# Kernel tuning notes

Measured on AMD Instinct MI355X. Metric: run time of the kernel, lower is better.

The kernel has to match this reference:

```python
import jax, jax.numpy as jnp
import numpy as np

E = 200_000   # edges (messages)
T = 2_000_000 # triplets
N = 20_000    # atoms/nodes
H = 128       # hidden_channels
INT = 64      # int_emb_size
BAS = 8       # basis_emb_size
OUT_EMB = 256 # out_emb_channels
NRAD = 6
SBF_DIM = 7 * 6  # num_spherical * num_radial = 42
NB = 4        # num_blocks
OUTC = 1      # num_targets


def setup_inputs() -> dict:
    key = jax.random.key(0)
    ks = iter(jax.random.split(key, 64))

    def w(shape):
        # glorot-ish scaled weights, stored as [in, out] for x @ W
        return jax.random.normal(next(ks), shape, jnp.float32) / np.sqrt(shape[-2])

    return dict(
        x=jax.random.normal(next(ks), (E, H), jnp.float32),
        rbf=jax.random.normal(next(ks), (E, NRAD), jnp.float32),
        sbf=jax.random.normal(next(ks), (T, SBF_DIM), jnp.float32),
        # interaction block params, stacked over NB blocks
        W_rbf1=w((NB, NRAD, BAS)), W_rbf2=w((NB, BAS, H)),
        W_sbf1=w((NB, SBF_DIM, BAS)), W_sbf2=w((NB, BAS, INT)),
        W_kj=w((NB, H, H)), b_kj=jnp.zeros((NB, H), jnp.float32),
        W_ji=w((NB, H, H)), b_ji=jnp.zeros((NB, H), jnp.float32),
        W_down=w((NB, H, INT)), W_up=w((NB, INT, H)),
        Wb=w((NB, 2, H, H)), bb=jnp.zeros((NB, 2, H), jnp.float32),   # num_before_skip=1 -> 2 linears
        Wa=w((NB, 4, H, H)), ba=jnp.zeros((NB, 4, H), jnp.float32),   # num_after_skip=2 -> 4 linears
        W_lin=w((NB, H, H)), b_lin=jnp.zeros((NB, H), jnp.float32),
        # output block params, stacked over NB+1 blocks
        Wo_rbf=w((NB + 1, NRAD, H)),
        Wo_up=w((NB + 1, H, OUT_EMB)), bo_up=jnp.zeros((NB + 1, OUT_EMB), jnp.float32),
        Wo_lins=w((NB + 1, 3, OUT_EMB, OUT_EMB)), bo_lins=jnp.zeros((NB + 1, 3, OUT_EMB), jnp.float32),
        Wo_out=w((NB + 1, OUT_EMB, OUTC)),
        idx_kj=jax.random.randint(next(ks), (T,), 0, E, jnp.int32),
        idx_ji=jax.random.randint(next(ks), (T,), 0, E, jnp.int32),
        idx_i=jax.random.randint(next(ks), (E,), 0, N, jnp.int32),
        num_nodes=N,
    )


def _interaction(b, x, rbf, sbf, idx_kj, idx_ji, p):
    act = jax.nn.silu
    x_ji = act(x @ p['W_ji'][b] + p['b_ji'][b])
    x_kj = act(x @ p['W_kj'][b] + p['b_kj'][b])
    rbf_t = (rbf @ p['W_rbf1'][b]) @ p['W_rbf2'][b]          # [E,H]
    x_kj = act((x_kj * rbf_t) @ p['W_down'][b])              # [E,INT]
    sbf_t = (sbf @ p['W_sbf1'][b]) @ p['W_sbf2'][b]          # [T,INT]
    m = x_kj[idx_kj] * sbf_t                                  # triplet gather [T,INT]
    agg = jax.ops.segment_sum(m, idx_ji, num_segments=x.shape[0])  # scatter-add [E,INT]
    x_kj = act(agg @ p['W_up'][b])                            # [E,H]
    h = x_ji + x_kj
    # residual layers before skip (1 layer = 2 linears)
    h = h + act(act(h @ p['Wb'][b, 0] + p['bb'][b, 0]) @ p['Wb'][b, 1] + p['bb'][b, 1])
    h = act(h @ p['W_lin'][b] + p['b_lin'][b]) + x
    # residual layers after skip (2 layers = 4 linears)
    for l in range(2):
        h = h + act(act(h @ p['Wa'][b, 2 * l] + p['ba'][b, 2 * l]) @ p['Wa'][b, 2 * l + 1] + p['ba'][b, 2 * l + 1])
    return h


def _output(b, x, rbf, idx_i, num_nodes, p):
    act = jax.nn.silu
    t = (rbf @ p['Wo_rbf'][b]) * x                            # [E,H]
    t = jax.ops.segment_sum(t, idx_i, num_segments=num_nodes) # [N,H]
    t = t @ p['Wo_up'][b] + p['bo_up'][b]
    for l in range(3):
        t = act(t @ p['Wo_lins'][b, l] + p['bo_lins'][b, l])
    return t @ p['Wo_out'][b]                                 # [N,OUTC]


def reference(x, rbf, sbf, W_rbf1, W_rbf2, W_sbf1, W_sbf2, W_kj, b_kj, W_ji, b_ji,
              W_down, W_up, Wb, bb, Wa, ba, W_lin, b_lin,
              Wo_rbf, Wo_up, bo_up, Wo_lins, bo_lins, Wo_out,
              idx_kj, idx_ji, idx_i, num_nodes):
    p = dict(W_rbf1=W_rbf1, W_rbf2=W_rbf2, W_sbf1=W_sbf1, W_sbf2=W_sbf2,
             W_kj=W_kj, b_kj=b_kj, W_ji=W_ji, b_ji=b_ji, W_down=W_down, W_up=W_up,
             Wb=Wb, bb=bb, Wa=Wa, ba=ba, W_lin=W_lin, b_lin=b_lin,
             Wo_rbf=Wo_rbf, Wo_up=Wo_up, bo_up=bo_up,
             Wo_lins=Wo_lins, bo_lins=bo_lins, Wo_out=Wo_out)
    P = _output(0, x, rbf, idx_i, num_nodes, p)
    for b in range(NB):  # fixed small layer loop
        x = _interaction(b, x, rbf, sbf, idx_kj, idx_ji, p)
        P = P + _output(b + 1, x, rbf, idx_i, num_nodes, p)
    return P
```

## Files before the change

### kernel.cpp

```cpp
#include <hip/hip_runtime.h>
#include <hip/hip_bf16.h>

#define E_EDGES 200000
#define T_TRIP  2000000
#define N_NODES 20000
#define H_DIM   128
#define INT_DIM 64
#define BAS     8
#define OUT_EMB 256
#define NRAD    6
#define SBF_D   42
#define NB      4

typedef __attribute__((ext_vector_type(8))) __bf16 bf16x8;
typedef __attribute__((ext_vector_type(4))) float f32x4;
typedef unsigned short u16;

__device__ __forceinline__ float silu_f(float v) { return v / (1.0f + __expf(-v)); }

__device__ __forceinline__ u16 f2bf(float f) {
    unsigned int u = __float_as_uint(f);
    u += 0x7FFF + ((u >> 16) & 1);
    return (u16)(u >> 16);
}
__device__ __forceinline__ float bf2f(u16 h) {
    return __uint_as_float(((unsigned int)h) << 16);
}

__device__ __forceinline__ void st_split4(char* H, char* L, int row, int col0, int stride,
                                          const float v[4]) {
    ushort4 hh, ll;
    u16 h0 = f2bf(v[0]); ll.x = f2bf(v[0] - bf2f(h0)); hh.x = h0;
    u16 h1 = f2bf(v[1]); ll.y = f2bf(v[1] - bf2f(h1)); hh.y = h1;
    u16 h2 = f2bf(v[2]); ll.z = f2bf(v[2] - bf2f(h2)); hh.z = h2;
    u16 h3 = f2bf(v[3]); ll.w = f2bf(v[3] - bf2f(h3)); hh.w = h3;
    int off = (row * stride + col0 * 2) ^ ((row & 7) << 4);
    *reinterpret_cast<ushort4*>(H + off) = hh;
    *reinterpret_cast<ushort4*>(L + off) = ll;
}
__device__ __forceinline__ void ld_split4(const char* H, const char* L, int row, int col0,
                                          int stride, float v[4]) {
    int off = (row * stride + col0 * 2) ^ ((row & 7) << 4);
    ushort4 hh = *reinterpret_cast<const ushort4*>(H + off);
    ushort4 ll = *reinterpret_cast<const ushort4*>(L + off);
    v[0] = bf2f(hh.x) + bf2f(ll.x);
    v[1] = bf2f(hh.y) + bf2f(ll.y);
    v[2] = bf2f(hh.z) + bf2f(ll.z);
    v[3] = bf2f(hh.w) + bf2f(ll.w);
}

struct BF8x4 { bf16x8 h[4]; bf16x8 l[4]; };

__device__ __forceinline__ BF8x4 loadB128f(const u16* __restrict__ Bh, const u16* __restrict__ Bl,
                                           int k0, int wn, int l15, int khalf)
{
    BF8x4 f;
    #pragma unroll
    for (int n = 0; n < 4; ++n) {
        size_t bo = (size_t)(wn * 64 + n * 16 + l15) * 128 + k0 + khalf;
        f.h[n] = *reinterpret_cast<const bf16x8*>(Bh + bo);
        f.l[n] = *reinterpret_cast<const bf16x8*>(Bl + bo);
    }
    return f;
}
__device__ __forceinline__ BF8x4 loadB64f(const u16* __restrict__ Bh, const u16* __restrict__ Bl,
                                          int k0, int wn, int l15, int khalf)
{
    BF8x4 f;
    #pragma unroll
    for (int n = 0; n < 4; ++n) {
        size_t bo = (size_t)(wn * 64 + n * 16 + l15) * 64 + k0 + khalf;
        f.h[n] = *reinterpret_cast<const bf16x8*>(Bh + bo);
        f.l[n] = *reinterpret_cast<const bf16x8*>(Bl + bo);
    }
    return f;
}
__device__ __forceinline__ BF8x4 loadB256f(const u16* __restrict__ Bh, const u16* __restrict__ Bl,
                                           int k0, int wn, int l15, int khalf)
{
    BF8x4 f;
    #pragma unroll
    for (int n = 0; n < 4; ++n) {
        size_t bo = (size_t)(wn * 64 + n * 16 + l15) * 256 + k0 + khalf;
        f.h[n] = *reinterpret_cast<const bf16x8*>(Bh + bo);
        f.l[n] = *reinterpret_cast<const bf16x8*>(Bl + bo);
    }
    return f;
}

__device__ __forceinline__ void mfma_cluster(
    const char* AH, const char* AL, int k0, int wm, int l15, int khalf,
    const BF8x4& b, f32x4 acc[2][4])
{
    __builtin_amdgcn_s_setprio(1);
    #pragma unroll
    for (int m = 0; m < 2; ++m) {
        int row = wm * 32 + m * 16 + l15;
        int off = (row * 256 + (k0 + khalf) * 2) ^ ((row & 7) << 4);
        bf16x8 ah = *reinterpret_cast<const bf16x8*>(AH + off);
        bf16x8 al = *reinterpret_cast<const bf16x8*>(AL + off);
        #pragma unroll
        for (int n = 0; n < 4; ++n) {
            acc[m][n] = __builtin_amdgcn_mfma_f32_16x16x32_bf16(b.h[n], ah, acc[m][n], 0, 0, 0);
            acc[m][n] = __builtin_amdgcn_mfma_f32_16x16x32_bf16(b.h[n], al, acc[m][n], 0, 0, 0);
            acc[m][n] = __builtin_amdgcn_mfma_f32_16x16x32_bf16(b.l[n], ah, acc[m][n], 0, 0, 0);
        }
    }
    __builtin_amdgcn_s_setprio(0);
}
__device__ __forceinline__ void mfma_cluster64(
    const char* AH, const char* AL, int k0, int wm, int l15, int khalf,
    const BF8x4& b, f32x4 acc[2][4])
{
    __builtin_amdgcn_s_setprio(1);
    #pragma unroll
    for (int m = 0; m < 2; ++m) {
        int row = wm * 32 + m * 16 + l15;
        int off = (row * 128 + (k0 + khalf) * 2) ^ ((row & 7) << 4);
        bf16x8 ah = *reinterpret_cast<const bf16x8*>(AH + off);
        bf16x8 al = *reinterpret_cast<const bf16x8*>(AL + off);
        #pragma unroll
        for (int n = 0; n < 4; ++n) {
            acc[m][n] = __builtin_amdgcn_mfma_f32_16x16x32_bf16(b.h[n], ah, acc[m][n], 0, 0, 0);
            acc[m][n] = __builtin_amdgcn_mfma_f32_16x16x32_bf16(b.h[n], al, acc[m][n], 0, 0, 0);
            acc[m][n] = __builtin_amdgcn_mfma_f32_16x16x32_bf16(b.l[n], ah, acc[m][n], 0, 0, 0);
        }
    }
    __builtin_amdgcn_s_setprio(0);
}
__device__ __forceinline__ void mfma_cluster512(
    const char* AH, const char* AL, int k0, int l15, int khalf,
    const BF8x4& b, f32x4 acc[2][4])
{
    __builtin_amdgcn_s_setprio(1);
    #pragma unroll
    for (int m = 0; m < 2; ++m) {
        int row = m * 16 + l15;
        int off = (row * 512 + (k0 + khalf) * 2) ^ ((row & 7) << 4);
        bf16x8 ah = *reinterpret_cast<const bf16x8*>(AH + off);
        bf16x8 al = *reinterpret_cast<const bf16x8*>(AL + off);
        #pragma unroll
        for (int n = 0; n < 4; ++n) {
            acc[m][n] = __builtin_amdgcn_mfma_f32_16x16x32_bf16(b.h[n], ah, acc[m][n], 0, 0, 0);
            acc[m][n] = __builtin_amdgcn_mfma_f32_16x16x32_bf16(b.h[n], al, acc[m][n], 0, 0, 0);
            acc[m][n] = __builtin_amdgcn_mfma_f32_16x16x32_bf16(b.l[n], ah, acc[m][n], 0, 0, 0);
        }
    }
    __builtin_amdgcn_s_setprio(0);
}

__device__ __forceinline__ void mm128_pipe(
    const char* AH, const char* AL,
    const u16* __restrict__ Bh, const u16* __restrict__ Bl, BF8x4& pre,
    const u16* __restrict__ nBh, const u16* __restrict__ nBl,
    int wm, int wn, int l15, int khalf, f32x4 acc[2][4])
{
    BF8x4 c0 = pre;
    BF8x4 c1 = loadB128f(Bh, Bl, 32, wn, l15, khalf);
    mfma_cluster(AH, AL, 0, wm, l15, khalf, c0, acc);
    BF8x4 c2 = loadB128f(Bh, Bl, 64, wn, l15, khalf);
    mfma_cluster(AH, AL, 32, wm, l15, khalf, c1, acc);
    BF8x4 c3 = loadB128f(Bh, Bl, 96, wn, l15, khalf);
    mfma_cluster(AH, AL, 64, wm, l15, khalf, c2, acc);
    if (nBh) pre = loadB128f(nBh, nBl, 0, wn, l15, khalf);
    mfma_cluster(AH, AL, 96, wm, l15, khalf, c3, acc);
}
__device__ __forceinline__ void mm64_pipe(
    const char* AH, const char* AL,
    const u16* __restrict__ Bh, const u16* __restrict__ Bl, BF8x4& pre,
    const u16* __restrict__ nBh, const u16* __restrict__ nBl,
    int wm, int wn, int l15, int khalf, f32x4 acc[2][4])
{
    BF8x4 c0 = pre;
    BF8x4 c1 = loadB64f(Bh, Bl, 32, wn, l15, khalf);
    mfma_cluster64(AH, AL, 0, wm, l15, khalf, c0, acc);
    if (nBh) pre = loadB128f(nBh, nBl, 0, wn, l15, khalf);
    mfma_cluster64(AH, AL, 32, wm, l15, khalf, c1, acc);
}

__global__ __launch_bounds__(256) void wprep(
    const float* __restrict__ src, u16* __restrict__ hi,
    u16* __restrict__ lo, int K, int N)
{
    int e = blockIdx.x * 256 + threadIdx.x;
    int total = K * N;
    if (e >= total) return;
    size_t base = (size_t)blockIdx.y * total;
    float a = src[base + e];
    int k = e / N, n = e - k * N;
    u16 h = f2bf(a);
    u16 l = f2bf(a - bf2f(h));
    hi[base + (size_t)n * K + k] = h;
    lo[base + (size_t)n * K + k] = l;
}

__global__ __launch_bounds__(256, 2) void pre_fuse(
    const float* __restrict__ X, const float* __restrict__ R8,
    const u16* __restrict__ Wjih, const u16* __restrict__ Wjil, const float* __restrict__ bji,
    const u16* __restrict__ Wkjh, const u16* __restrict__ Wkjl, const float* __restrict__ bkj,
    const float* __restrict__ Wr2,
    const u16* __restrict__ Wdnh, const u16* __restrict__ Wdnl,
    float* __restrict__ E1, float* __restrict__ C1)
{
    __shared__ u16 XH[64 * 128], XL[64 * 128];
    __shared__ u16 IH[64 * 128], IL[64 * 128];

    const int tid  = threadIdx.x;
    const int lane = tid & 63;
    const int w    = tid >> 6;
    const int wm   = w >> 1, wn = w & 1;
    const int bm   = blockIdx.x * 64;
    const int l15  = lane & 15;
    const int khalf = (lane >> 4) * 8;
    const int r4   = (lane >> 4) * 4;

    BF8x4 pre = loadB128f(Wjih, Wjil, 0, wn, l15, khalf);

    {
        int r  = tid >> 2;
        int c0 = (tid & 3) * 32;
        const float* p = &X[(size_t)(bm + r) * H_DIM + c0];
        const int swz = (r & 7) << 4;
        #pragma unroll
        for (int q = 0; q < 8; ++q) {
            float4 f = *reinterpret_cast<const float4*>(p + q * 4);
            float vv[4] = {f.x, f.y, f.z, f.w};
            u16 h[4], l[4];
            #pragma unroll
            for (int j = 0; j < 4; ++j) {
                h[j] = f2bf(vv[j]);
                l[j] = f2bf(vv[j] - bf2f(h[j]));
            }
            int off = (r * 256 + c0 * 2 + q * 8) ^ swz;
            *reinterpret_cast<ushort4*>((char*)XH + off) = make_ushort4(h[0], h[1], h[2], h[3]);
            *reinterpret_cast<ushort4*>((char*)XL + off) = make_ushort4(l[0], l[1], l[2], l[3]);
        }
    }
    __syncthreads();

    {
        f32x4 acc[2][4] = {};
        mm128_pipe((char*)XH, (char*)XL, Wjih, Wjil, pre, Wkjh, Wkjl,
                   wm, wn, l15, khalf, acc);
        #pragma unroll
        for (int n = 0; n < 4; ++n) {
            int col0 = wn * 64 + n * 16 + r4;
            float4 bv = *reinterpret_cast<const float4*>(&bji[col0]);
            #pragma unroll
            for (int m = 0; m < 2; ++m) {
                int row = wm * 32 + m * 16 + l15;
                float4 o;
                o.x = silu_f(acc[m][n][0] + bv.x);
                o.y = silu_f(acc[m][n][1] + bv.y);
                o.z = silu_f(acc[m][n][2] + bv.z);
                o.w = silu_f(acc[m][n][3] + bv.w);
                *reinterpret_cast<float4*>(&E1[(size_t)(bm + row) * H_DIM + col0]) = o;
            }
        }
    }
    {
        f32x4 acc[2][4] = {};
        mm128_pipe((char*)XH, (char*)XL, Wkjh, Wkjl, pre, nullptr, nullptr,
                   wm, wn, l15, khalf, acc);
        float r8v[2][8];
        #pragma unroll
        for (int m = 0; m < 2; ++m) {
            int grow = bm + wm * 32 + m * 16 + l15;
            const float4* rp = reinterpret_cast<const float4*>(&R8[(size_t)grow * 8]);
            float4 a = rp[0], b2 = rp[1];
            r8v[m][0] = a.x;  r8v[m][1] = a.y;  r8v[m][2] = a.z;  r8v[m][3] = a.w;
            r8v[m][4] = b2.x; r8v[m][5] = b2.y; r8v[m][6] = b2.z; r8v[m][7] = b2.w;
        }
        #pragma unroll
        for (int n = 0; n < 4; ++n) {
            int col0 = wn * 64 + n * 16 + r4;
            float4 bvf = *reinterpret_cast<const float4*>(&bkj[col0]);
            float bv[4] = {bvf.x, bvf.y, bvf.z, bvf.w};
            float wrv[8][4];
            #pragma unroll
            for (int j = 0; j < 8; ++j) {
                float4 wf = *reinterpret_cast<const float4*>(&Wr2[j * H_DIM + col0]);
                wrv[j][0] = wf.x; wrv[j][1] = wf.y; wrv[j][2] = wf.z; wrv[j][3] = wf.w;
            }
            #pragma unroll
            for (int m = 0; m < 2; ++m) {
                int row = wm * 32 + m * 16 + l15;
                float v[4];
                #pragma unroll
                for (int r = 0; r < 4; ++r) {
                    float t = silu_f(acc[m][n][r] + bv[r]);
                    float g = 0.f;
                    #pragma unroll
                    for (int j = 0; j < 8; ++j)
                        g = fmaf(r8v[m][j], wrv[j][r], g);
                    v[r] = t * g;
                }
                st_split4((char*)IH, (char*)IL, row, col0, 256, v);
            }
        }
    }
    __syncthreads();

    {
        f32x4 acc[2][2] = {};
        #pragma unroll
        for (int k0 = 0; k0 < 128; k0 += 32) {
            bf16x8 bh[2], bl[2];
            #pragma unroll
            for (int n = 0; n < 2; ++n) {
                size_t bo = (size_t)(wn * 32 + n * 16 + l15) * 128 + k0 + khalf;
                bh[n] = *reinterpret_cast<const bf16x8*>(Wdnh + bo);
                bl[n] = *reinterpret_cast<const bf16x8*>(Wdnl + bo);
            }
            __builtin_amdgcn_s_setprio(1);
            #pragma unroll
            for (int m = 0; m < 2; ++m) {
                int row = wm * 32 + m * 16 + l15;
                int off = (row * 256 + (k0 + khalf) * 2) ^ ((row & 7) << 4);
                bf16x8 ah = *reinterpret_cast<const bf16x8*>((const char*)IH + off);
                bf16x8 al = *reinterpret_cast<const bf16x8*>((const char*)IL + off);
                #pragma unroll
                for (int n = 0; n < 2; ++n) {
                    acc[m][n] = __builtin_amdgcn_mfma_f32_16x16x32_bf16(bh[n], ah, acc[m][n], 0, 0, 0);
                    acc[m][n] = __builtin_amdgcn_mfma_f32_16x16x32_bf16(bh[n], al, acc[m][n], 0, 0, 0);
                    acc[m][n] = __builtin_amdgcn_mfma_f32_16x16x32_bf16(bl[n], ah, acc[m][n], 0, 0, 0);
                }
            }
            __builtin_amdgcn_s_setprio(0);
        }
        #pragma unroll
        for (int n = 0; n < 2; ++n) {
            int col0 = wn * 32 + n * 16 + r4;
            #pragma unroll
            for (int m = 0; m < 2; ++m) {
                int row = wm * 32 + m * 16 + l15;
                float4 o;
                o.x = silu_f(acc[m][n][0]);
                o.y = silu_f(acc[m][n][1]);
                o.z = silu_f(acc[m][n][2]);
                o.w = silu_f(acc[m][n][3]);
                *reinterpret_cast<float4*>(&C1[(size_t)(bm + row) * INT_DIM + col0]) = o;
            }
        }
    }
}

struct ChainP {
    const u16 *uph, *upl;
    const u16 *b0h, *b0l, *b1h, *b1l;
    const u16 *lnh, *lnl;
    const u16 *a0h, *a0l, *a1h, *a1l, *a2h, *a2l, *a3h, *a3l;
    const float *bb0, *bb1, *blin, *ba0, *ba1, *ba2, *ba3;
};

__global__ __launch_bounds__(256, 2) void post_chain(
    const float* __restrict__ AGG, const float* __restrict__ E1,
    const float* __restrict__ X, ChainP p, float* __restrict__ OUT)
{
    __shared__ u16 GH[64 * 64],  GL[64 * 64];
    __shared__ u16 P0H[64 * 128], P0L[64 * 128];
    __shared__ u16 P1H[64 * 128], P1L[64 * 128];

    const int tid  = threadIdx.x;
    const int lane = tid & 63;
    const int w    = tid >> 6;
    const int wm   = w >> 1, wn = w & 1;
    const int bm   = blockIdx.x * 64;
    const int l15  = lane & 15;
    const int khalf = (lane >> 4) * 8;
    const int r4   = (lane >> 4) * 4;

    BF8x4 pre = loadB64f(p.uph, p.upl, 0, wn, l15, khalf);

    {
        int r  = tid >> 2;
        int c0 = (tid & 3) * 16;
        const float* pg = &AGG[(size_t)(bm + r) * INT_DIM + c0];
        const int swz = (r & 7) << 4;
        #pragma unroll
        for (int q = 0; q < 4; ++q) {
            float4 f = *reinterpret_cast<const float4*>(pg + q * 4);
            float vv[4] = {f.x, f.y, f.z, f.w};
            u16 h[4], l[4];
            #pragma unroll
            for (int j = 0; j < 4; ++j) {
                h[j] = f2bf(vv[j]);
                l[j] = f2bf(vv[j] - bf2f(h[j]));
            }
            int off = (r * 128 + c0 * 2 + q * 8) ^ swz;
            *reinterpret_cast<ushort4*>((char*)GH + off) = make_ushort4(h[0], h[1], h[2], h[3]);
            *reinterpret_cast<ushort4*>((char*)GL + off) = make_ushort4(l[0], l[1], l[2], l[3]);
        }
    }
    __syncthreads();

    f32x4 acc[2][4];

    #pragma unroll
    for (int m = 0; m < 2; ++m)
        #pragma unroll
        for (int n = 0; n < 4; ++n) acc[m][n] = f32x4{0.f, 0.f, 0.f, 0.f};
    mm64_pipe((char*)GH, (char*)GL, p.uph, p.upl, pre, p.b0h, p.b0l,
              wm, wn, l15, khalf, acc);
    #pragma unroll
    for (int n = 0; n < 4; ++n) {
        int col0 = wn * 64 + n * 16 + r4;
        #pragma unroll
        for (int m = 0; m < 2; ++m) {
            int row = wm * 32 + m * 16 + l15;
            float4 e = *reinterpret_cast<const float4*>(&E1[(size_t)(bm + row) * H_DIM + col0]);
            float v[4];
            v[0] = e.x + silu_f(acc[m][n][0]);
            v[1] = e.y + silu_f(acc[m][n][1]);
            v[2] = e.z + silu_f(acc[m][n][2]);
            v[3] = e.w + silu_f(acc[m][n][3]);
            st_split4((char*)P0H, (char*)P0L, row, col0, 256, v);
        }
    }
    __syncthreads();

    #define STAGE_PLAIN(SRC_H, SRC_L, WH, WL, BIAS, DST_H, DST_L, NWH, NWL)             \
    {                                                                                   \
        _Pragma("unroll")                                                               \
        for (int m = 0; m < 2; ++m)                                                     \
            _Pragma("unroll")                                                           \
            for (int n = 0; n < 4; ++n) acc[m][n] = f32x4{0.f, 0.f, 0.f, 0.f};          \
        mm128_pipe((char*)SRC_H, (char*)SRC_L, WH, WL, pre, NWH, NWL,                   \
                   wm, wn, l15, khalf, acc);                                            \
        _Pragma("unroll")                                                               \
        for (int n = 0; n < 4; ++n) {                                                   \
            int col0 = wn * 64 + n * 16 + r4;                                           \
            float4 bv = *reinterpret_cast<const float4*>(&BIAS[col0]);                  \
            _Pragma("unroll")                                                           \
            for (int m = 0; m < 2; ++m) {                                               \
                int row = wm * 32 + m * 16 + l15;                                       \
                float v[4];                                                             \
                v[0] = silu_f(acc[m][n][0] + bv.x);                                     \
                v[1] = silu_f(acc[m][n][1] + bv.y);                                     \
                v[2] = silu_f(acc[m][n][2] + bv.z);                                     \
                v[3] = silu_f(acc[m][n][3] + bv.w);                                     \
                st_split4((char*)DST_H, (char*)DST_L, row, col0, 256, v);               \
            }                                                                           \
        }                                                                               \
        __syncthreads();                                                                \
    }

    #define STAGE_RES(SRC_H, SRC_L, WH, WL, BIAS, RES_H, RES_L, NWH, NWL)               \
    {                                                                                   \
        _Pragma("unroll")                                                               \
        for (int m = 0; m < 2; ++m)                                                     \
            _Pragma("unroll")                                                           \
            for (int n = 0; n < 4; ++n) acc[m][n] = f32x4{0.f, 0.f, 0.f, 0.f};          \
        mm128_pipe((char*)SRC_H, (char*)SRC_L, WH, WL, pre, NWH, NWL,                   \
                   wm, wn, l15, khalf, acc);                                            \
        _Pragma("unroll")                                                               \
        for (int n = 0; n < 4; ++n) {                                                   \
            int col0 = wn * 64 + n * 16 + r4;                                           \
            float4 bv = *reinterpret_cast<const float4*>(&BIAS[col0]);                  \
            _Pragma("unroll")                                                           \
            for (int m = 0; m < 2; ++m) {                                               \
                int row = wm * 32 + m * 16 + l15;                                       \
                float v[4];                                                             \
                ld_split4((char*)RES_H, (char*)RES_L, row, col0, 256, v);               \
                v[0] += silu_f(acc[m][n][0] + bv.x);                                    \
                v[1] += silu_f(acc[m][n][1] + bv.y);                                    \
                v[2] += silu_f(acc[m][n][2] + bv.z);                                    \
                v[3] += silu_f(acc[m][n][3] + bv.w);                                    \
                st_split4((char*)RES_H, (char*)RES_L, row, col0, 256, v);               \
            }                                                                           \
        }                                                                               \
        __syncthreads();                                                                \
    }

    STAGE_PLAIN(P0H, P0L, p.b0h, p.b0l, p.bb0, P1H, P1L, p.b1h, p.b1l)
    STAGE_RES(P1H, P1L, p.b1h, p.b1l, p.bb1, P0H, P0L, p.lnh, p.lnl)

    {
        #pragma unroll
        for (int m = 0; m < 2; ++m)
            #pragma unroll
            for (int n = 0; n < 4; ++n) acc[m][n] = f32x4{0.f, 0.f, 0.f, 0.f};
        mm128_pipe((char*)P0H, (char*)P0L, p.lnh, p.lnl, pre, p.a0h, p.a0l,
                   wm, wn, l15, khalf, acc);
        #pragma unroll
        for (int n = 0; n < 4; ++n) {
            int col0 = wn * 64 + n * 16 + r4;
            float4 bv = *reinterpret_cast<const float4*>(&p.blin[col0]);
            #pragma unroll
            for (int m = 0; m < 2; ++m) {
                int row = wm * 32 + m * 16 + l15;
                float4 xv = *reinterpret_cast<const float4*>(&X[(size_t)(bm + row) * H_DIM + col0]);
                float v[4];
                v[0] = silu_f(acc[m][n][0] + bv.x) + xv.x;
                v[1] = silu_f(acc[m][n][1] + bv.y) + xv.y;
                v[2] = silu_f(acc[m][n][2] + bv.z) + xv.z;
                v[3] = silu_f(acc[m][n][3] + bv.w) + xv.w;
                st_split4((char*)P1H, (char*)P1L, row, col0, 256, v);
            }
        }
        __syncthreads();
    }

    STAGE_PLAIN(P1H, P1L, p.a0h, p.a0l, p.ba0, P0H, P0L, p.a1h, p.a1l)
    STAGE_RES(P0H, P0L, p.a1h, p.a1l, p.ba1, P1H, P1L, p.a2h, p.a2l)
    STAGE_PLAIN(P1H, P1L, p.a2h, p.a2l, p.ba2, P0H, P0L, p.a3h, p.a3l)

    {
        #pragma unroll
        for (int m = 0; m < 2; ++m)
            #pragma unroll
            for (int n = 0; n < 4; ++n) acc[m][n] = f32x4{0.f, 0.f, 0.f, 0.f};
        mm128_pipe((char*)P0H, (char*)P0L, p.a3h, p.a3l, pre, nullptr, nullptr,
                   wm, wn, l15, khalf, acc);
        #pragma unroll
        for (int n = 0; n < 4; ++n) {
            int col0 = wn * 64 + n * 16 + r4;
            float4 bv = *reinterpret_cast<const float4*>(&p.ba3[col0]);
            #pragma unroll
            for (int m = 0; m < 2; ++m) {
                int row = wm * 32 + m * 16 + l15;
                float v[4];
                ld_split4((char*)P1H, (char*)P1L, row, col0, 256, v);
                float4 o;
                o.x = v[0] + silu_f(acc[m][n][0] + bv.x);
                o.y = v[1] + silu_f(acc[m][n][1] + bv.y);
                o.z = v[2] + silu_f(acc[m][n][2] + bv.z);
                o.w = v[3] + silu_f(acc[m][n][3] + bv.w);
                *reinterpret_cast<float4*>(&OUT[(size_t)(bm + row) * H_DIM + col0]) = o;
            }
        }
    }
    #undef STAGE_PLAIN
    #undef STAGE_RES
}

__global__ __launch_bounds__(256, 2) void out_chain(
    const float* __restrict__ TN,
    const u16* __restrict__ Uh, const u16* __restrict__ Ul, const float* __restrict__ bu,
    const u16* __restrict__ L0h, const u16* __restrict__ L0l, const float* __restrict__ b0,
    const u16* __restrict__ L1h, const u16* __restrict__ L1l, const float* __restrict__ b1,
    const u16* __restrict__ L2h, const u16* __restrict__ L2l, const float* __restrict__ b2,
    const float* __restrict__ Wo, float* __restrict__ P)
{
    __shared__ u16 XH[32 * 128], XL[32 * 128];
    __shared__ u16 T0H[32 * 256], T0L[32 * 256];
    __shared__ u16 T1H[32 * 256], T1L[32 * 256];

    const int tid  = threadIdx.x;
    const int lane = tid & 63;
    const int wn   = tid >> 6;
    const int bm   = blockIdx.x * 32;
    const int l15  = lane & 15;
    const int khalf = (lane >> 4) * 8;
    const int r4   = (lane >> 4) * 4;

    {
        int r  = tid >> 3;
        int c0 = (tid & 7) * 16;
        const float* p = &TN[(size_t)(bm + r) * H_DIM + c0];
        const int swz = (r & 7) << 4;
        #pragma unroll
        for (int q = 0; q < 4; ++q) {
            float4 f = *reinterpret_cast<const float4*>(p + q * 4);
            float vv[4] = {f.x, f.y, f.z, f.w};
            u16 h[4], l[4];
            #pragma unroll
            for (int j = 0; j < 4; ++j) {
                h[j] = f2bf(vv[j]);
                l[j] = f2bf(vv[j] - bf2f(h[j]));
            }
            int off = (r * 256 + c0 * 2 + q * 8) ^ swz;
            *reinterpret_cast<ushort4*>((char*)XH + off) = make_ushort4(h[0], h[1], h[2], h[3]);
            *reinterpret_cast<ushort4*>((char*)XL + off) = make_ushort4(l[0], l[1], l[2], l[3]);
        }
    }
    __syncthreads();

    f32x4 acc[2][4];

    {
        #pragma unroll
        for (int m = 0; m < 2; ++m)
            #pragma unroll
            for (int n = 0; n < 4; ++n) acc[m][n] = f32x4{0.f, 0.f, 0.f, 0.f};
        BF8x4 cur = loadB128f(Uh, Ul, 0, wn, l15, khalf);
        #pragma unroll
        for (int k = 0; k < 4; ++k) {
            BF8x4 nxt;
            if (k < 3) nxt = loadB128f(Uh, Ul, 32 * (k + 1), wn, l15, khalf);
            mfma_cluster((char*)XH, (char*)XL, 32 * k, 0, l15, khalf, cur, acc);
            if (k < 3) cur = nxt;
        }
        #pragma unroll
        for (int n = 0; n < 4; ++n) {
            int col0 = wn * 64 + n * 16 + r4;
            float4 bv = *reinterpret_cast<const float4*>(&bu[col0]);
            #pragma unroll
            for (int m = 0; m < 2; ++m) {
                int row = m * 16 + l15;
                float v[4] = {acc[m][n][0] + bv.x, acc[m][n][1] + bv.y,
                              acc[m][n][2] + bv.z, acc[m][n][3] + bv.w};
                st_split4((char*)T0H, (char*)T0L, row, col0, 512, v);
            }
        }
        __syncthreads();
    }

    #define OLIN(SRC_H, SRC_L, WH, WL, BIAS, DST_H, DST_L)                              \
    {                                                                                   \
        _Pragma("unroll")                                                               \
        for (int m = 0; m < 2; ++m)                                                     \
            _Pragma("unroll")                                                           \
            for (int n = 0; n < 4; ++n) acc[m][n] = f32x4{0.f, 0.f, 0.f, 0.f};          \
        BF8x4 cur = loadB256f(WH, WL, 0, wn, l15, khalf);                               \
        _Pragma("unroll")                                                               \
        for (int k = 0; k < 8; ++k) {                                                   \
            BF8x4 nxt;                                                                  \
            if (k < 7) nxt = loadB256f(WH, WL, 32 * (k + 1), wn, l15, khalf);           \
            mfma_cluster512((char*)SRC_H, (char*)SRC_L, 32 * k, l15, khalf, cur, acc);  \
            if (k < 7) cur = nxt;                                                       \
        }                                                                               \
        _Pragma("unroll")                                                               \
        for (int n = 0; n < 4; ++n) {                                                   \
            int col0 = wn * 64 + n * 16 + r4;                                           \
            float4 bv = *reinterpret_cast<const float4*>(&BIAS[col0]);                  \
            _Pragma("unroll")                                                           \
            for (int m = 0; m < 2; ++m) {                                               \
                int row = m * 16 + l15;                                                 \
                float v[4];                                                             \
                v[0] = silu_f(acc[m][n][0] + bv.x);                                     \
                v[1] = silu_f(acc[m][n][1] + bv.y);                                     \
                v[2] = silu_f(acc[m][n][2] + bv.z);                                     \
                v[3] = silu_f(acc[m][n][3] + bv.w);                                     \
                st_split4((char*)DST_H, (char*)DST_L, row, col0, 512, v);               \
            }                                                                           \
        }                                                                               \
        __syncthreads();                                                                \
    }

    OLIN(T0H, T0L, L0h, L0l, b0, T1H, T1L)
    OLIN(T1H, T1L, L1h, L1l, b1, T0H, T0L)
    OLIN(T0H, T0L, L2h, L2l, b2, T1H, T1L)
    #undef OLIN

    {
        int row  = tid >> 3;
        int part = tid & 7;
        float s = 0.f;
        int cbase = part * 32;
        #pragma unroll
        for (int c4 = 0; c4 < 32; c4 += 4) {
            float v[4];
            ld_split4((char*)T1H, (char*)T1L, row, cbase + c4, 512, v);
            float4 wv = *reinterpret_cast<const float4*>(&Wo[cbase + c4]);
            s = fmaf(v[0], wv.x, s);
            s = fmaf(v[1], wv.y, s);
            s = fmaf(v[2], wv.z, s);
            s = fmaf(v[3], wv.w, s);
        }
        s += __shfl_xor(s, 1);
        s += __shfl_xor(s, 2);
        s += __shfl_xor(s, 4);
        if (part == 0) P[bm + row] += s;
    }
}

__global__ __launch_bounds__(256) void rbf8_kernel(
    const float* __restrict__ rbf, const float* __restrict__ W1,
    float* __restrict__ r8, int Ecount)
{
    int e = blockIdx.x * blockDim.x + threadIdx.x;
    if (e >= Ecount) return;
    float rv[NRAD];
    #pragma unroll
    for (int k = 0; k < NRAD; ++k) rv[k] = rbf[(size_t)e * NRAD + k];
    float acc[BAS] = {};
    #pragma unroll
    for (int k = 0; k < NRAD; ++k)
        #pragma unroll
        for (int j = 0; j < BAS; ++j)
            acc[j] = fmaf(rv[k], W1[k * BAS + j], acc[j]);
    float4* o = reinterpret_cast<float4*>(&r8[(size_t)e * BAS]);
    o[0] = make_float4(acc[0], acc[1], acc[2], acc[3]);
    o[1] = make_float4(acc[4], acc[5], acc[6], acc[7]);
}

__global__ __launch_bounds__(256) void csr_count(
    const int* __restrict__ idx, int* __restrict__ cnt, int n)
{
    int i = blockIdx.x * 256 + threadIdx.x;
    if (i < n) atomicAdd(&cnt[idx[i]], 1);
}

__global__ __launch_bounds__(256) void scan_block(
    const int* __restrict__ cnt, int* __restrict__ ptr, int* __restrict__ bsum, int n)
{
    __shared__ int s[256];
    int i = blockIdx.x * 256 + threadIdx.x;
    int v = (i < n) ? cnt[i] : 0;
    s[threadIdx.x] = v;
    __syncthreads();
    #pragma unroll
    for (int off = 1; off < 256; off <<= 1) {
        int t = (threadIdx.x >= off) ? s[threadIdx.x - off] : 0;
        __syncthreads();
        s[threadIdx.x] += t;
        __syncthreads();
    }
    if (i < n) ptr[i] = s[threadIdx.x] - v;
    if (threadIdx.x == 255) bsum[blockIdx.x] = s[255];
}

__global__ __launch_bounds__(1024) void scan_aux(int* __restrict__ bsum, int nb)
{
    __shared__ int s[1024];
    int v = (threadIdx.x < nb) ? bsum[threadIdx.x] : 0;
    s[threadIdx.x] = v;
    __syncthreads();
    #pragma unroll
    for (int off = 1; off < 1024; off <<= 1) {
        int t = (threadIdx.x >= off) ? s[threadIdx.x - off] : 0;
        __syncthreads();
        s[threadIdx.x] += t;
        __syncthreads();
    }
    if (threadIdx.x < nb) bsum[threadIdx.x] = s[threadIdx.x] - v;
}

__global__ __launch_bounds__(256) void scan_add(
    int* __restrict__ ptr, const int* __restrict__ bsum, int n)
{
    int i = blockIdx.x * 256 + threadIdx.x;
    if (i < n) ptr[i] += bsum[blockIdx.x];
}

__global__ __launch_bounds__(256) void csr_fill(
    const int* __restrict__ idx, int* __restrict__ cursor,
    int* __restrict__ perm, int n)
{
    int i = blockIdx.x * 256 + threadIdx.x;
    if (i >= n) return;
    int pos = atomicAdd(&cursor[idx[i]], 1);
    perm[pos] = i;
}

__global__ __launch_bounds__(256) void permute_s8(
    const float* __restrict__ sbf, const float* __restrict__ W1all,
    const int* __restrict__ idx_kj, const int* __restrict__ tperm,
    u16* __restrict__ ps8, int* __restrict__ pkj, int Tcount)
{
    __shared__ float Ws[NB * SBF_D * BAS];
    for (int i = threadIdx.x; i < NB * SBF_D * BAS; i += 256) Ws[i] = W1all[i];
    __syncthreads();
    int i = blockIdx.x * 256 + threadIdx.x;
    if (i >= Tcount) return;
    int t = tperm[i];
    pkj[i] = idx_kj[t];
    float s[SBF_D];
    {
        const float2* p2 = reinterpret_cast<const float2*>(&sbf[(size_t)t * SBF_D]);
        #pragma unroll
        for (int k = 0; k < SBF_D / 2; ++k) {
            float2 v = p2[k];
            s[2 * k] = v.x; s[2 * k + 1] = v.y;
        }
    }
    #pragma unroll
    for (int b = 0; b < NB; ++b) {
        const float* Wb_ = &Ws[b * SBF_D * BAS];
        float acc[BAS] = {};
        for (int k = 0; k < SBF_D; ++k) {
            float sv = s[k];
            #pragma unroll
            for (int j = 0; j < BAS; ++j)
                acc[j] = fmaf(sv, Wb_[k * BAS + j], acc[j]);
        }
        ushort4 o0 = make_ushort4(f2bf(acc[0]), f2bf(acc[1]), f2bf(acc[2]), f2bf(acc[3]));
        ushort4 o1 = make_ushort4(f2bf(acc[4]), f2bf(acc[5]), f2bf(acc[6]), f2bf(acc[7]));
        u16* op = &ps8[((size_t)b * Tcount + i) * BAS];
        *reinterpret_cast<ushort4*>(op) = o0;
        *reinterpret_cast<ushort4*>(op + 4) = o1;
    }
}

__device__ __forceinline__ float dot8_bf(uint4 r, const float* w2) {
    float s;
    s  = bf2f((u16)(r.x)) * w2[0] + bf2f((u16)(r.x >> 16)) * w2[1];
    s += bf2f((u16)(r.y)) * w2[2] + bf2f((u16)(r.y >> 16)) * w2[3];
    s += bf2f((u16)(r.z)) * w2[4] + bf2f((u16)(r.z >> 16)) * w2[5];
    s += bf2f((u16)(r.w)) * w2[6] + bf2f((u16)(r.w >> 16)) * w2[7];
    return s;
}

__global__ __launch_bounds__(256) void triplet_gather2(
    const u16* __restrict__ ps8b, const float* __restrict__ Wsb2,
    const float* __restrict__ xkj, const int* __restrict__ pkj,
    const int* __restrict__ tptr, const int* __restrict__ tcnt,
    float* __restrict__ agg, int Ecount)
{
    const int lane = threadIdx.x & 63;
    int wid = (blockIdx.x * blockDim.x + threadIdx.x) >> 6;
    const int nw = (gridDim.x * blockDim.x) >> 6;
    float w2[BAS];
    #pragma unroll
    for (int j = 0; j < BAS; ++j) w2[j] = Wsb2[j * INT_DIM + lane];

    for (int e = wid; e < Ecount; e += nw) {
        int start = tptr[e];
        int end   = start + tcnt[e];
        float acc0 = 0.f, acc1 = 0.f;
        int i = start;
        for (; i + 1 < end; i += 2) {
            uint4 ra = *reinterpret_cast<const uint4*>(&ps8b[(size_t)i * BAS]);
            uint4 rb = *reinterpret_cast<const uint4*>(&ps8b[(size_t)(i + 1) * BAS]);
            int e0 = pkj[i], e1 = pkj[i + 1];
            float s0 = dot8_bf(ra, w2);
            float s1 = dot8_bf(rb, w2);
            acc0 = fmaf(xkj[(size_t)e0 * INT_DIM + lane], s0, acc0);
            acc1 = fmaf(xkj[(size_t)e1 * INT_DIM + lane], s1, acc1);
        }
        if (i < end) {
            uint4 ra = *reinterpret_cast<const uint4*>(&ps8b[(size_t)i * BAS]);
            int e0 = pkj[i];
            acc0 = fmaf(xkj[(size_t)e0 * INT_DIM + lane], dot8_bf(ra, w2), acc0);
        }
        agg[(size_t)e * INT_DIM + lane] = acc0 + acc1;
    }
}

__global__ __launch_bounds__(256) void out_gather(
    const float* __restrict__ rbf, const float* __restrict__ Wor,
    const float* __restrict__ x,
    const int* __restrict__ eptr, const int* __restrict__ ecnt,
    const int* __restrict__ eperm, float* __restrict__ tN, int Nn)
{
    const int lane = threadIdx.x & 63;
    int wid = (blockIdx.x * blockDim.x + threadIdx.x) >> 6;
    const int nw = (gridDim.x * blockDim.x) >> 6;
    float wr0[NRAD], wr1[NRAD];
    #pragma unroll
    for (int k = 0; k < NRAD; ++k) {
        wr0[k] = Wor[k * H_DIM + lane];
        wr1[k] = Wor[k * H_DIM + lane + 64];
    }
    for (int n = wid; n < Nn; n += nw) {
        int start = eptr[n];
        int end   = start + ecnt[n];
        float a0 = 0.f, a1 = 0.f;
        for (int i = start; i < end; ++i) {
            int e = eperm[i];
            const float2* rp = reinterpret_cast<const float2*>(&rbf[(size_t)e * NRAD]);
            float2 r0 = rp[0], r1 = rp[1], r2 = rp[2];
            float rA = r0.x*wr0[0] + r0.y*wr0[1] + r1.x*wr0[2]
                     + r1.y*wr0[3] + r2.x*wr0[4] + r2.y*wr0[5];
            float rB = r0.x*wr1[0] + r0.y*wr1[1] + r1.x*wr1[2]
                     + r1.y*wr1[3] + r2.x*wr1[4] + r2.y*wr1[5];
            a0 = fmaf(rA, x[(size_t)e * H_DIM + lane], a0);
            a1 = fmaf(rB, x[(size_t)e * H_DIM + lane + 64], a1);
        }
        tN[(size_t)n * H_DIM + lane] = a0;
        tN[(size_t)n * H_DIM + lane + 64] = a1;
    }
}

extern "C" void kernel_launch(void* const* d_in, const int* in_sizes, int n_in,
                              void* d_out, int out_size, void* d_ws, size_t ws_size,
                              hipStream_t stream)
{
    const float* x_in    = (const float*)d_in[0];
    const float* rbf     = (const float*)d_in[1];
    const float* sbf     = (const float*)d_in[2];
    const float* W_rbf1  = (const float*)d_in[3];
    const float* W_rbf2  = (const float*)d_in[4];
    const float* W_sbf1  = (const float*)d_in[5];
    const float* W_sbf2  = (const float*)d_in[6];
    const float* W_kj    = (const float*)d_in[7];
    const float* b_kj    = (const float*)d_in[8];
    const float* W_ji    = (const float*)d_in[9];
    const float* b_ji    = (const float*)d_in[10];
    const float* W_down  = (const float*)d_in[11];
    const float* W_up    = (const float*)d_in[12];
    const float* Wb      = (const float*)d_in[13];
    const float* bb      = (const float*)d_in[14];
    const float* Wa      = (const float*)d_in[15];
    const float* ba      = (const float*)d_in[16];
    const float* W_lin   = (const float*)d_in[17];
    const float* b_lin   = (const float*)d_in[18];
    const float* Wo_rbf  = (const float*)d_in[19];
    const float* Wo_up   = (const float*)d_in[20];
    const float* bo_up   = (const float*)d_in[21];
    const float* Wo_lins = (const float*)d_in[22];
    const float* bo_lins = (const float*)d_in[23];
    const float* Wo_out  = (const float*)d_in[24];
    const int*   idx_kj  = (const int*)d_in[25];
    const int*   idx_ji  = (const int*)d_in[26];
    const int*   idx_i   = (const int*)d_in[27];

    char* ws = (char*)d_ws;
    size_t off = 0;
    auto alloc = [&](size_t bytes) -> void* {
        void* p = (void*)(ws + off);
        off += (bytes + 255) & ~(size_t)255;
        return p;
    };
    float* XA = (float*)alloc((size_t)E_EDGES * H_DIM * 4);
    float* XB = (float*)alloc((size_t)E_EDGES * H_DIM * 4);
    float* E1 = (float*)alloc((size_t)E_EDGES * H_DIM * 4);
    float* C1 = (float*)alloc((size_t)E_EDGES * INT_DIM * 4);
    float* C2 = (float*)alloc((size_t)E_EDGES * INT_DIM * 4);
    float* R8 = (float*)alloc((size_t)E_EDGES * BAS * 4);
    float* TN = (float*)alloc((size_t)N_NODES * H_DIM * 4);
    u16* HKJ = (u16*)alloc(4  * 16384 * 2); u16* LKJ = (u16*)alloc(4  * 16384 * 2);
    u16* HJI = (u16*)alloc(4  * 16384 * 2); u16* LJI = (u16*)alloc(4  * 16384 * 2);
    u16* HDN = (u16*)alloc(4  * 8192  * 2); u16* LDN = (u16*)alloc(4  * 8192  * 2);
    u16* HUP = (u16*)alloc(4  * 8192  * 2); u16* LUP = (u16*)alloc(4  * 8192  * 2);
    u16* HWB = (u16*)alloc(8  * 16384 * 2); u16* LWB = (u16*)alloc(8  * 16384 * 2);
    u16* HWA = (u16*)alloc(16 * 16384 * 2); u16* LWA = (u16*)alloc(16 * 16384 * 2);
    u16* HLN = (u16*)alloc(4  * 16384 * 2); u16* LLN = (u16*)alloc(4  * 16384 * 2);
    u16* HOU = (u16*)alloc(5  * 32768 * 2); u16* LOU = (u16*)alloc(5  * 32768 * 2);
    u16* HOL = (u16*)alloc(15 * 65536 * 2); u16* LOL = (u16*)alloc(15 * 65536 * 2);
    int* tcnt  = (int*)alloc((size_t)E_EDGES * 4);
    int* tptr  = (int*)alloc((size_t)E_EDGES * 4);
    int* tcur  = (int*)alloc((size_t)E_EDGES * 4);
    int* tperm = (int*)alloc((size_t)T_TRIP * 4);
    int* tbsum = (int*)alloc(1024 * 4);
    int* ecnt  = (int*)alloc((size_t)N_NODES * 4);
    int* eptr  = (int*)alloc((size_t)N_NODES * 4);
    int* ecur  = (int*)alloc((size_t)N_NODES * 4);
    int* eperm = (int*)alloc((size_t)E_EDGES * 4);
    int* ebsum = (int*)alloc(1024 * 4);
    u16* PS8 = (u16*)alloc((size_t)NB * T_TRIP * BAS * 2);
    int* PKJ = (int*)alloc((size_t)T_TRIP * 4);
    (void)ws_size;

    auto prep = [&](const float* src, u16* hi, u16* lo, int K, int N, int cnt) {
        dim3 g((K * N + 255) / 256, cnt);
        hipLaunchKernelGGL(wprep, g, dim3(256), 0, stream, src, hi, lo, K, N);
    };
    prep(W_kj,    HKJ, LKJ, 128, 128, 4);
    prep(W_ji,    HJI, LJI, 128, 128, 4);
    prep(W_down,  HDN, LDN, 128, 64,  4);
    prep(W_up,    HUP, LUP, 64,  128, 4);
    prep(Wb,      HWB, LWB, 128, 128, 8);
    prep(Wa,      HWA, LWA, 128, 128, 16);
    prep(W_lin,   HLN, LLN, 128, 128, 4);
    prep(Wo_up,   HOU, LOU, 128, 256, 5);
    prep(Wo_lins, HOL, LOL, 256, 256, 15);

    {
        const int nbT = (E_EDGES + 255) / 256;
        hipMemsetAsync(tcnt, 0, (size_t)E_EDGES * 4, stream);
        hipLaunchKernelGGL(csr_count, dim3((T_TRIP + 255) / 256), dim3(256), 0, stream,
                           idx_ji, tcnt, T_TRIP);
        hipLaunchKernelGGL(scan_block, dim3(nbT), dim3(256), 0, stream, tcnt, tptr, tbsum, E_EDGES);
        hipLaunchKernelGGL(scan_aux, dim3(1), dim3(1024), 0, stream, tbsum, nbT);
        hipLaunchKernelGGL(scan_add, dim3(nbT), dim3(256), 0, stream, tptr, tbsum, E_EDGES);
        hipMemcpyAsync(tcur, tptr, (size_t)E_EDGES * 4, hipMemcpyDeviceToDevice, stream);
        hipLaunchKernelGGL(csr_fill, dim3((T_TRIP + 255) / 256), dim3(256), 0, stream,
                           idx_ji, tcur, tperm, T_TRIP);
    }
    {
        const int nbN = (N_NODES + 255) / 256;
        hipMemsetAsync(ecnt, 0, (size_t)N_NODES * 4, stream);
        hipLaunchKernelGGL(csr_count, dim3((E_EDGES + 255) / 256), dim3(256), 0, stream,
                           idx_i, ecnt, E_EDGES);
        hipLaunchKernelGGL(scan_block, dim3(nbN), dim3(256), 0, stream, ecnt, eptr, ebsum, N_NODES);
        hipLaunchKernelGGL(scan_aux, dim3(1), dim3(1024), 0, stream, ebsum, nbN);
        hipLaunchKernelGGL(scan_add, dim3(nbN), dim3(256), 0, stream, eptr, ebsum, N_NODES);
        hipMemcpyAsync(ecur, eptr, (size_t)N_NODES * 4, hipMemcpyDeviceToDevice, stream);
        hipLaunchKernelGGL(csr_fill, dim3((E_EDGES + 255) / 256), dim3(256), 0, stream,
                           idx_i, ecur, eperm, E_EDGES);
    }
    hipLaunchKernelGGL(permute_s8, dim3((T_TRIP + 255) / 256), dim3(256), 0, stream,
                       sbf, W_sbf1, idx_kj, tperm, PS8, PKJ, T_TRIP);

    float* P = (float*)d_out;
    hipMemsetAsync(P, 0, (size_t)N_NODES * sizeof(float), stream);

    auto out_block = [&](int ob, const float* xcur) {
        hipLaunchKernelGGL(out_gather, dim3(2048), dim3(256), 0, stream,
                           rbf, Wo_rbf + (size_t)ob * NRAD * H_DIM, xcur,
                           eptr, ecnt, eperm, TN, N_NODES);
        hipLaunchKernelGGL(out_chain, dim3(N_NODES / 32), dim3(256), 0, stream,
                           TN,
                           HOU + (size_t)ob * 32768, LOU + (size_t)ob * 32768,
                           bo_up + (size_t)ob * OUT_EMB,
                           HOL + (size_t)(ob * 3 + 0) * 65536, LOL + (size_t)(ob * 3 + 0) * 65536,
                           bo_lins + (size_t)(ob * 3 + 0) * OUT_EMB,
                           HOL + (size_t)(ob * 3 + 1) * 65536, LOL + (size_t)(ob * 3 + 1) * 65536,
                           bo_lins + (size_t)(ob * 3 + 1) * OUT_EMB,
                           HOL + (size_t)(ob * 3 + 2) * 65536, LOL + (size_t)(ob * 3 + 2) * 65536,
                           bo_lins + (size_t)(ob * 3 + 2) * OUT_EMB,
                           Wo_out + (size_t)ob * OUT_EMB, P);
    };

    out_block(0, x_in);

    const float* xcur = x_in;
    const int EB = E_EDGES / 64;
    for (int b = 0; b < NB; ++b) {
        float* xnext = (b % 2 == 0) ? XB : XA;
        hipLaunchKernelGGL(rbf8_kernel, dim3((E_EDGES + 255) / 256), dim3(256), 0, stream,
                           rbf, W_rbf1 + (size_t)b * NRAD * BAS, R8, E_EDGES);
        hipLaunchKernelGGL(pre_fuse, dim3(EB), dim3(256), 0, stream,
                           xcur, R8,
                           HJI + (size_t)b * 16384, LJI + (size_t)b * 16384, b_ji + (size_t)b * H_DIM,
                           HKJ + (size_t)b * 16384, LKJ + (size_t)b * 16384, b_kj + (size_t)b * H_DIM,
                           W_rbf2 + (size_t)b * BAS * H_DIM,
                           HDN + (size_t)b * 8192, LDN + (size_t)b * 8192,
                           E1, C1);
        hipLaunchKernelGGL(triplet_gather2, dim3(2048), dim3(256), 0, stream,
                           PS8 + (size_t)b * T_TRIP * BAS, W_sbf2 + (size_t)b * BAS * INT_DIM,
                           C1, PKJ, tptr, tcnt, C2, E_EDGES);
        ChainP cp;
        cp.uph = HUP + (size_t)b * 8192;  cp.upl = LUP + (size_t)b * 8192;
        cp.b0h = HWB + (size_t)(b * 2 + 0) * 16384; cp.b0l = LWB + (size_t)(b * 2 + 0) * 16384;
        cp.b1h = HWB + (size_t)(b * 2 + 1) * 16384; cp.b1l = LWB + (size_t)(b * 2 + 1) * 16384;
        cp.lnh = HLN + (size_t)b * 16384; cp.lnl = LLN + (size_t)b * 16384;
        cp.a0h = HWA + (size_t)(b * 4 + 0) * 16384; cp.a0l = LWA + (size_t)(b * 4 + 0) * 16384;
        cp.a1h = HWA + (size_t)(b * 4 + 1) * 16384; cp.a1l = LWA + (size_t)(b * 4 + 1) * 16384;
        cp.a2h = HWA + (size_t)(b * 4 + 2) * 16384; cp.a2l = LWA + (size_t)(b * 4 + 2) * 16384;
        cp.a3h = HWA + (size_t)(b * 4 + 3) * 16384; cp.a3l = LWA + (size_t)(b * 4 + 3) * 16384;
        cp.bb0 = bb + (size_t)(b * 2 + 0) * H_DIM;
        cp.bb1 = bb + (size_t)(b * 2 + 1) * H_DIM;
        cp.blin = b_lin + (size_t)b * H_DIM;
        cp.ba0 = ba + (size_t)(b * 4 + 0) * H_DIM;
        cp.ba1 = ba + (size_t)(b * 4 + 1) * H_DIM;
        cp.ba2 = ba + (size_t)(b * 4 + 2) * H_DIM;
        cp.ba3 = ba + (size_t)(b * 4 + 3) * H_DIM;
        hipLaunchKernelGGL(post_chain, dim3(EB), dim3(256), 0, stream,
                           C2, E1, xcur, cp, xnext);
        xcur = xnext;
        out_block(b + 1, xcur);
    }
}
```

Measured before the change: 4.372 ms.

## Fuse output-block kernels into interaction gather and chain launches via block partitioning

Folds the rbf8 projection into pre_fuse so the per-edge R8 buffer and its launch disappear. The output block for the previous x (node gather and node MLP chain) now runs inside the same grids as the triplet gather and the edge post-chain, with block index ranges split between the two jobs and shared memory given as a raw byte buffer. This cuts launch count and lets the independent output-block work fill idle CUs alongside the interaction work. The fused kernels carry the larger shared-memory footprint and register use of both bodies, which may lower occupancy.

```diff
diff --git a/kernel.cpp b/kernel.cpp
--- a/kernel.cpp
+++ b/kernel.cpp
@@ -195,7 +195,8 @@
 }
 
 __global__ __launch_bounds__(256, 2) void pre_fuse(
-    const float* __restrict__ X, const float* __restrict__ R8,
+    const float* __restrict__ X, const float* __restrict__ rbf,
+    const float* __restrict__ W1,
     const u16* __restrict__ Wjih, const u16* __restrict__ Wjil, const float* __restrict__ bji,
     const u16* __restrict__ Wkjh, const u16* __restrict__ Wkjl, const float* __restrict__ bkj,
     const float* __restrict__ Wr2,
@@ -266,10 +267,16 @@
         #pragma unroll
         for (int m = 0; m < 2; ++m) {
             int grow = bm + wm * 32 + m * 16 + l15;
-            const float4* rp = reinterpret_cast<const float4*>(&R8[(size_t)grow * 8]);
-            float4 a = rp[0], b2 = rp[1];
-            r8v[m][0] = a.x;  r8v[m][1] = a.y;  r8v[m][2] = a.z;  r8v[m][3] = a.w;
-            r8v[m][4] = b2.x; r8v[m][5] = b2.y; r8v[m][6] = b2.z; r8v[m][7] = b2.w;
+            const float2* rp = reinterpret_cast<const float2*>(&rbf[(size_t)grow * NRAD]);
+            float2 q0 = rp[0], q1 = rp[1], q2 = rp[2];
+            float rv[NRAD] = {q0.x, q0.y, q1.x, q1.y, q2.x, q2.y};
+            #pragma unroll
+            for (int j = 0; j < 8; ++j) r8v[m][j] = 0.f;
+            #pragma unroll
+            for (int k = 0; k < NRAD; ++k)
+                #pragma unroll
+                for (int j = 0; j < 8; ++j)
+                    r8v[m][j] = fmaf(rv[k], W1[k * BAS + j], r8v[m][j]);
         }
         #pragma unroll
         for (int n = 0; n < 4; ++n) {
@@ -352,20 +359,32 @@
     const u16 *a0h, *a0l, *a1h, *a1l, *a2h, *a2l, *a3h, *a3l;
     const float *bb0, *bb1, *blin, *ba0, *ba1, *ba2, *ba3;
 };
-
-__global__ __launch_bounds__(256, 2) void post_chain(
+struct OutP {
+    const float* TN;
+    const u16 *Uh, *Ul; const float* bu;
+    const u16 *L0h, *L0l; const float* b0;
+    const u16 *L1h, *L1l; const float* b1;
+    const u16 *L2h, *L2l; const float* b2;
+    const float* Wo; float* P;
+};
+
+__device__ __forceinline__ void post_chain_body(
+    char* smem, int bx,
     const float* __restrict__ AGG, const float* __restrict__ E1,
-    const float* __restrict__ X, ChainP p, float* __restrict__ OUT)
-{
-    __shared__ u16 GH[64 * 64],  GL[64 * 64];
-    __shared__ u16 P0H[64 * 128], P0L[64 * 128];
-    __shared__ u16 P1H[64 * 128], P1L[64 * 128];
+    const float* __restrict__ X, const ChainP& p, float* __restrict__ OUT)
+{
+    char* GH  = smem;
+    char* GL  = smem + 8192;
+    char* P0H = smem + 16384;
+    char* P0L = smem + 32768;
+    char* P1H = smem + 49152;
+    char* P1L = smem + 65536;
 
     const int tid  = threadIdx.x;
     const int lane = tid & 63;
     const int w    = tid >> 6;
     const int wm   = w >> 1, wn = w & 1;
-    const int bm   = blockIdx.x * 64;
+    const int bm   = bx * 64;
     const int l15  = lane & 15;
     const int khalf = (lane >> 4) * 8;
     const int r4   = (lane >> 4) * 4;
@@ -388,8 +407,8 @@
                 l[j] = f2bf(vv[j] - bf2f(h[j]));
             }
             int off = (r * 128 + c0 * 2 + q * 8) ^ swz;
-            *reinterpret_cast<ushort4*>((char*)GH + off) = make_ushort4(h[0], h[1], h[2], h[3]);
-            *reinterpret_cast<ushort4*>((char*)GL + off) = make_ushort4(l[0], l[1], l[2], l[3]);
+            *reinterpret_cast<ushort4*>(GH + off) = make_ushort4(h[0], h[1], h[2], h[3]);
+            *reinterpret_cast<ushort4*>(GL + off) = make_ushort4(l[0], l[1], l[2], l[3]);
         }
     }
     __syncthreads();
@@ -400,8 +419,7 @@
     for (int m = 0; m < 2; ++m)
         #pragma unroll
         for (int n = 0; n < 4; ++n) acc[m][n] = f32x4{0.f, 0.f, 0.f, 0.f};
-    mm64_pipe((char*)GH, (char*)GL, p.uph, p.upl, pre, p.b0h, p.b0l,
-              wm, wn, l15, khalf, acc);
+    mm64_pipe(GH, GL, p.uph, p.upl, pre, p.b0h, p.b0l, wm, wn, l15, khalf, acc);
     #pragma unroll
     for (int n = 0; n < 4; ++n) {
         int col0 = wn * 64 + n * 16 + r4;
@@ -414,7 +432,7 @@
             v[1] = e.y + silu_f(acc[m][n][1]);
             v[2] = e.z + silu_f(acc[m][n][2]);
             v[3] = e.w + silu_f(acc[m][n][3]);
-            st_split4((char*)P0H, (char*)P0L, row, col0, 256, v);
+            st_split4(P0H, P0L, row, col0, 256, v);
         }
     }
     __syncthreads();
@@ -425,8 +443,7 @@
         for (int m = 0; m < 2; ++m)                                                     \
             _Pragma("unroll")                                                           \
             for (int n = 0; n < 4; ++n) acc[m][n] = f32x4{0.f, 0.f, 0.f, 0.f};          \
-        mm128_pipe((char*)SRC_H, (char*)SRC_L, WH, WL, pre, NWH, NWL,                   \
-                   wm, wn, l15, khalf, acc);                                            \
+        mm128_pipe(SRC_H, SRC_L, WH, WL, pre, NWH, NWL, wm, wn, l15, khalf, acc);       \
         _Pragma("unroll")                                                               \
         for (int n = 0; n < 4; ++n) {                                                   \
             int col0 = wn * 64 + n * 16 + r4;                                           \
@@ -439,7 +456,7 @@
                 v[1] = silu_f(acc[m][n][1] + bv.y);                                     \
                 v[2] = silu_f(acc[m][n][2] + bv.z);                                     \
                 v[3] = silu_f(acc[m][n][3] + bv.w);                                     \
-                st_split4((char*)DST_H, (char*)DST_L, row, col0, 256, v);               \
+                st_split4(DST_H, DST_L, row, col0, 256, v);                             \
             }                                                                           \
         }                                                                               \
         __syncthreads();                                                                \
@@ -451,8 +468,7 @@
         for (int m = 0; m < 2; ++m)                                                     \
             _Pragma("unroll")                                                           \
             for (int n = 0; n < 4; ++n) acc[m][n] = f32x4{0.f, 0.f, 0.f, 0.f};          \
-        mm128_pipe((char*)SRC_H, (char*)SRC_L, WH, WL, pre, NWH, NWL,                   \
-                   wm, wn, l15, khalf, acc);                                            \
+        mm128_pipe(SRC_H, SRC_L, WH, WL, pre, NWH, NWL, wm, wn, l15, khalf, acc);       \
         _Pragma("unroll")                                                               \
         for (int n = 0; n < 4; ++n) {                                                   \
             int col0 = wn * 64 + n * 16 + r4;                                           \
@@ -461,12 +477,12 @@
             for (int m = 0; m < 2; ++m) {                                               \
                 int row = wm * 32 + m * 16 + l15;                                       \
                 float v[4];                                                             \
-                ld_split4((char*)RES_H, (char*)RES_L, row, col0, 256, v);               \
+                ld_split4(RES_H, RES_L, row, col0, 256, v);                             \
                 v[0] += silu_f(acc[m][n][0] + bv.x);                                    \
                 v[1] += silu_f(acc[m][n][1] + bv.y);                                    \
                 v[2] += silu_f(acc[m][n][2] + bv.z);                                    \
                 v[3] += silu_f(acc[m][n][3] + bv.w);                                    \
-                st_split4((char*)RES_H, (char*)RES_L, row, col0, 256, v);               \
+                st_split4(RES_H, RES_L, row, col0, 256, v);                             \
             }                                                                           \
         }                                                                               \
         __syncthreads();                                                                \
@@ -480,8 +496,7 @@
         for (int m = 0; m < 2; ++m)
             #pragma unroll
             for (int n = 0; n < 4; ++n) acc[m][n] = f32x4{0.f, 0.f, 0.f, 0.f};
-        mm128_pipe((char*)P0H, (char*)P0L, p.lnh, p.lnl, pre, p.a0h, p.a0l,
-                   wm, wn, l15, khalf, acc);
+        mm128_pipe(P0H, P0L, p.lnh, p.lnl, pre, p.a0h, p.a0l, wm, wn, l15, khalf, acc);
         #pragma unroll
         for (int n = 0; n < 4; ++n) {
             int col0 = wn * 64 + n * 16 + r4;
@@ -495,7 +510,7 @@
                 v[1] = silu_f(acc[m][n][1] + bv.y) + xv.y;
                 v[2] = silu_f(acc[m][n][2] + bv.z) + xv.z;
                 v[3] = silu_f(acc[m][n][3] + bv.w) + xv.w;
-                st_split4((char*)P1H, (char*)P1L, row, col0, 256, v);
+                st_split4(P1H, P1L, row, col0, 256, v);
             }
         }
         __syncthreads();
@@ -510,8 +525,7 @@
         for (int m = 0; m < 2; ++m)
             #pragma unroll
             for (int n = 0; n < 4; ++n) acc[m][n] = f32x4{0.f, 0.f, 0.f, 0.f};
-        mm128_pipe((char*)P0H, (char*)P0L, p.a3h, p.a3l, pre, nullptr, nullptr,
-                   wm, wn, l15, khalf, acc);
+        mm128_pipe(P0H, P0L, p.a3h, p.a3l, pre, nullptr, nullptr, wm, wn, l15, khalf, acc);
         #pragma unroll
         for (int n = 0; n < 4; ++n) {
             int col0 = wn * 64 + n * 16 + r4;
@@ -520,7 +534,7 @@
             for (int m = 0; m < 2; ++m) {
                 int row = wm * 32 + m * 16 + l15;
                 float v[4];
-                ld_split4((char*)P1H, (char*)P1L, row, col0, 256, v);
+                ld_split4(P1H, P1L, row, col0, 256, v);
                 float4 o;
                 o.x = v[0] + silu_f(acc[m][n][0] + bv.x);
                 o.y = v[1] + silu_f(acc[m][n][1] + bv.y);
@@ -534,22 +548,19 @@
     #undef STAGE_RES
 }
 
-__global__ __launch_bounds__(256, 2) void out_chain(
-    const float* __restrict__ TN,
-    const u16* __restrict__ Uh, const u16* __restrict__ Ul, const float* __restrict__ bu,
-    const u16* __restrict__ L0h, const u16* __restrict__ L0l, const float* __restrict__ b0,
-    const u16* __restrict__ L1h, const u16* __restrict__ L1l, const float* __restrict__ b1,
-    const u16* __restrict__ L2h, const u16* __restrict__ L2l, const float* __restrict__ b2,
-    const float* __restrict__ Wo, float* __restrict__ P)
-{
-    __shared__ u16 XH[32 * 128], XL[32 * 128];
-    __shared__ u16 T0H[32 * 256], T0L[32 * 256];
-    __shared__ u16 T1H[32 * 256], T1L[32 * 256];
+__device__ __forceinline__ void out_chain_body(char* smem, int bx, const OutP& o)
+{
+    char* XH  = smem;
+    char* XL  = smem + 8192;
+    char* T0H = smem + 16384;
+    char* T0L = smem + 32768;
+    char* T1H = smem + 49152;
+    char* T1L = smem + 65536;
 
     const int tid  = threadIdx.x;
     const int lane = tid & 63;
     const int wn   = tid >> 6;
-    const int bm   = blockIdx.x * 32;
+    const int bm   = bx * 32;
     const int l15  = lane & 15;
     const int khalf = (lane >> 4) * 8;
     const int r4   = (lane >> 4) * 4;
@@ -557,7 +568,7 @@
     {
         int r  = tid >> 3;
         int c0 = (tid & 7) * 16;
-        const float* p = &TN[(size_t)(bm + r) * H_DIM + c0];
+        const float* p = &o.TN[(size_t)(bm + r) * H_DIM + c0];
         const int swz = (r & 7) << 4;
         #pragma unroll
         for (int q = 0; q < 4; ++q) {
@@ -570,8 +581,8 @@
                 l[j] = f2bf(vv[j] - bf2f(h[j]));
             }
             int off = (r * 256 + c0 * 2 + q * 8) ^ swz;
-            *reinterpret_cast<ushort4*>((char*)XH + off) = make_ushort4(h[0], h[1], h[2], h[3]);
-            *reinterpret_cast<ushort4*>((char*)XL + off) = make_ushort4(l[0], l[1], l[2], l[3]);
+            *reinterpret_cast<ushort4*>(XH + off) = make_ushort4(h[0], h[1], h[2], h[3]);
+            *reinterpret_cast<ushort4*>(XL + off) = make_ushort4(l[0], l[1], l[2], l[3]);
         }
     }
     __syncthreads();
@@ -583,24 +594,24 @@
         for (int m = 0; m < 2; ++m)
             #pragma unroll
             for (int n = 0; n < 4; ++n) acc[m][n] = f32x4{0.f, 0.f, 0.f, 0.f};
-        BF8x4 cur = loadB128f(Uh, Ul, 0, wn, l15, khalf);
+        BF8x4 cur = loadB128f(o.Uh, o.Ul, 0, wn, l15, khalf);
         #pragma unroll
         for (int k = 0; k < 4; ++k) {
             BF8x4 nxt;
-            if (k < 3) nxt = loadB128f(Uh, Ul, 32 * (k + 1), wn, l15, khalf);
-            mfma_cluster((char*)XH, (char*)XL, 32 * k, 0, l15, khalf, cur, acc);
+            if (k < 3) nxt = loadB128f(o.Uh, o.Ul, 32 * (k + 1), wn, l15, khalf);
+            mfma_cluster(XH, XL, 32 * k, 0, l15, khalf, cur, acc);
             if (k < 3) cur = nxt;
         }
         #pragma unroll
         for (int n = 0; n < 4; ++n) {
             int col0 = wn * 64 + n * 16 + r4;
-            float4 bv = *reinterpret_cast<const float4*>(&bu[col0]);
+            float4 bv = *reinterpret_cast<const float4*>(&o.bu[col0]);
             #pragma unroll
             for (int m = 0; m < 2; ++m) {
                 int row = m * 16 + l15;
                 float v[4] = {acc[m][n][0] + bv.x, acc[m][n][1] + bv.y,
                               acc[m][n][2] + bv.z, acc[m][n][3] + bv.w};
-                st_split4((char*)T0H, (char*)T0L, row, col0, 512, v);
+                st_split4(T0H, T0L, row, col0, 512, v);
             }
         }
         __syncthreads();
@@ -617,7 +628,7 @@
         for (int k = 0; k < 8; ++k) {                                                   \
             BF8x4 nxt;                                                                  \
             if (k < 7) nxt = loadB256f(WH, WL, 32 * (k + 1), wn, l15, khalf);           \
-            mfma_cluster512((char*)SRC_H, (char*)SRC_L, 32 * k, l15, khalf, cur, acc);  \
+            mfma_cluster512(SRC_H, SRC_L, 32 * k, l15, khalf, cur, acc);                \
             if (k < 7) cur = nxt;                                                       \
         }                                                                               \
         _Pragma("unroll")                                                               \
@@ -632,15 +643,15 @@
                 v[1] = silu_f(acc[m][n][1] + bv.y);                                     \
                 v[2] = silu_f(acc[m][n][2] + bv.z);                                     \
                 v[3] = silu_f(acc[m][n][3] + bv.w);                                     \
-                st_split4((char*)DST_H, (char*)DST_L, row, col0, 512, v);               \
+                st_split4(DST_H, DST_L, row, col0, 512, v);                             \
             }                                                                           \
         }                                                                               \
         __syncthreads();                                                                \
     }
 
-    OLIN(T0H, T0L, L0h, L0l, b0, T1H, T1L)
-    OLIN(T1H, T1L, L1h, L1l, b1, T0H, T0L)
-    OLIN(T0H, T0L, L2h, L2l, b2, T1H, T1L)
+    OLIN(T0H, T0L, o.L0h, o.L0l, o.b0, T1H, T1L)
+    OLIN(T1H, T1L, o.L1h, o.L1l, o.b1, T0H, T0L)
+    OLIN(T0H, T0L, o.L2h, o.L2l, o.b2, T1H, T1L)
     #undef OLIN
 
     {
@@ -651,8 +662,8 @@
         #pragma unroll
         for (int c4 = 0; c4 < 32; c4 += 4) {
             float v[4];
-            ld_split4((char*)T1H, (char*)T1L, row, cbase + c4, 512, v);
-            float4 wv = *reinterpret_cast<const float4*>(&Wo[cbase + c4]);
+            ld_split4(T1H, T1L, row, cbase + c4, 512, v);
+            float4 wv = *reinterpret_cast<const float4*>(&o.Wo[cbase + c4]);
             s = fmaf(v[0], wv.x, s);
             s = fmaf(v[1], wv.y, s);
             s = fmaf(v[2], wv.z, s);
@@ -661,126 +672,20 @@
         s += __shfl_xor(s, 1);
         s += __shfl_xor(s, 2);
         s += __shfl_xor(s, 4);
-        if (part == 0) P[bm + row] += s;
-    }
-}
-
-__global__ __launch_bounds__(256) void rbf8_kernel(
-    const float* __restrict__ rbf, const float* __restrict__ W1,
-    float* __restrict__ r8, int Ecount)
-{
-    int e = blockIdx.x * blockDim.x + threadIdx.x;
-    if (e >= Ecount) return;
-    float rv[NRAD];
-    #pragma unroll
-    for (int k = 0; k < NRAD; ++k) rv[k] = rbf[(size_t)e * NRAD + k];
-    float acc[BAS] = {};
-    #pragma unroll
-    for (int k = 0; k < NRAD; ++k)
-        #pragma unroll
-        for (int j = 0; j < BAS; ++j)
-            acc[j] = fmaf(rv[k], W1[k * BAS + j], acc[j]);
-    float4* o = reinterpret_cast<float4*>(&r8[(size_t)e * BAS]);
-    o[0] = make_float4(acc[0], acc[1], acc[2], acc[3]);
-    o[1] = make_float4(acc[4], acc[5], acc[6], acc[7]);
-}
-
-__global__ __launch_bounds__(256) void csr_count(
-    const int* __restrict__ idx, int* __restrict__ cnt, int n)
-{
-    int i = blockIdx.x * 256 + threadIdx.x;
-    if (i < n) atomicAdd(&cnt[idx[i]], 1);
-}
-
-__global__ __launch_bounds__(256) void scan_block(
-    const int* __restrict__ cnt, int* __restrict__ ptr, int* __restrict__ bsum, int n)
-{
-    __shared__ int s[256];
-    int i = blockIdx.x * 256 + threadIdx.x;
-    int v = (i < n) ? cnt[i] : 0;
-    s[threadIdx.x] = v;
-    __syncthreads();
-    #pragma unroll
-    for (int off = 1; off < 256; off <<= 1) {
-        int t = (threadIdx.x >= off) ? s[threadIdx.x - off] : 0;
-        __syncthreads();
-        s[threadIdx.x] += t;
-        __syncthreads();
-    }
-    if (i < n) ptr[i] = s[threadIdx.x] - v;
-    if (threadIdx.x == 255) bsum[blockIdx.x] = s[255];
-}
-
-__global__ __launch_bounds__(1024) void scan_aux(int* __restrict__ bsum, int nb)
-{
-    __shared__ int s[1024];
-    int v = (threadIdx.x < nb) ? bsum[threadIdx.x] : 0;
-    s[threadIdx.x] = v;
-    __syncthreads();
-    #pragma unroll
-    for (int off = 1; off < 1024; off <<= 1) {
-        int t = (threadIdx.x >= off) ? s[threadIdx.x - off] : 0;
-        __syncthreads();
-        s[threadIdx.x] += t;
-        __syncthreads();
-    }
-    if (threadIdx.x < nb) bsum[threadIdx.x] = s[threadIdx.x] - v;
-}
-
-__global__ __launch_bounds__(256) void scan_add(
-    int* __restrict__ ptr, const int* __restrict__ bsum, int n)
-{
-    int i = blockIdx.x * 256 + threadIdx.x;
-    if (i < n) ptr[i] += bsum[blockIdx.x];
-}
-
-__global__ __launch_bounds__(256) void csr_fill(
-    const int* __restrict__ idx, int* __restrict__ cursor,
-    int* __restrict__ perm, int n)
-{
-    int i = blockIdx.x * 256 + threadIdx.x;
-    if (i >= n) return;
-    int pos = atomicAdd(&cursor[idx[i]], 1);
-    perm[pos] = i;
-}
-
-__global__ __launch_bounds__(256) void permute_s8(
-    const float* __restrict__ sbf, const float* __restrict__ W1all,
-    const int* __restrict__ idx_kj, const int* __restrict__ tperm,
-    u16* __restrict__ ps8, int* __restrict__ pkj, int Tcount)
-{
-    __shared__ float Ws[NB * SBF_D * BAS];
-    for (int i = threadIdx.x; i < NB * SBF_D * BAS; i += 256) Ws[i] = W1all[i];
-    __syncthreads();
-    int i = blockIdx.x * 256 + threadIdx.x;
-    if (i >= Tcount) return;
-    int t = tperm[i];
-    pkj[i] = idx_kj[t];
-    float s[SBF_D];
-    {
-        const float2* p2 = reinterpret_cast<const float2*>(&sbf[(size_t)t * SBF_D]);
-        #pragma unroll
-        for (int k = 0; k < SBF_D / 2; ++k) {
-            float2 v = p2[k];
-            s[2 * k] = v.x; s[2 * k + 1] = v.y;
-        }
-    }
-    #pragma unroll
-    for (int b = 0; b < NB; ++b) {
-        const float* Wb_ = &Ws[b * SBF_D * BAS];
-        float acc[BAS] = {};
-        for (int k = 0; k < SBF_D; ++k) {
-            float sv = s[k];
-            #pragma unroll
-            for (int j = 0; j < BAS; ++j)
-                acc[j] = fmaf(sv, Wb_[k * BAS + j], acc[j]);
-        }
-        ushort4 o0 = make_ushort4(f2bf(acc[0]), f2bf(acc[1]), f2bf(acc[2]), f2bf(acc[3]));
-        ushort4 o1 = make_ushort4(f2bf(acc[4]), f2bf(acc[5]), f2bf(acc[6]), f2bf(acc[7]));
-        u16* op = &ps8[((size_t)b * Tcount + i) * BAS];
-        *reinterpret_cast<ushort4*>(op) = o0;
-        *reinterpret_cast<ushort4*>(op + 4) = o1;
-    }
+        if (part == 0) o.P[bm + row] += s;
+    }
+}
+
+__global__ __launch_bounds__(256, 2) void post_fused(
+    int npost,
+    const float* __restrict__ AGG, const float* __restrict__ E1,
+    const float* __restrict__ X, ChainP p, float* __restrict__ OUT, OutP o)
+{
+    __shared__ char smem[81920];
+    if ((int)blockIdx.x < npost)
+        post_chain_body(smem, blockIdx.x, AGG, E1, X, p, OUT);
+    else
+        out_chain_body(smem, blockIdx.x - npost, o);
 }
 
 __device__ __forceinline__ float dot8_bf(uint4 r, const float* w2) {
@@ -792,20 +697,21 @@
     return s;
 }
 
-__global__ __launch_bounds__(256) void triplet_gather2(
+__device__ __forceinline__ void triplet_body(
+    int bx, int nblk,
     const u16* __restrict__ ps8b, const float* __restrict__ Wsb2,
     const float* __restrict__ xkj, const int* __restrict__ pkj,
     const int* __restrict__ tptr, const int* __restrict__ tcnt,
-    float* __restrict__ agg, int Ecount)
+    float* __restrict__ agg)
 {
     const int lane = threadIdx.x & 63;
-    int wid = (blockIdx.x * blockDim.x + threadIdx.x) >> 6;
-    const int nw = (gridDim.x * blockDim.x) >> 6;
+    int wid = bx * 4 + (threadIdx.x >> 6);
+    const int nw = nblk * 4;
     float w2[BAS];
     #pragma unroll
     for (int j = 0; j < BAS; ++j) w2[j] = Wsb2[j * INT_DIM + lane];
 
-    for (int e = wid; e < Ecount; e += nw) {
+    for (int e = wid; e < E_EDGES; e += nw) {
         int start = tptr[e];
         int end   = start + tcnt[e];
         float acc0 = 0.f, acc1 = 0.f;
@@ -828,22 +734,23 @@
     }
 }
 
-__global__ __launch_bounds__(256) void out_gather(
+__device__ __forceinline__ void out_gather_body(
+    int bx, int nblk,
     const float* __restrict__ rbf, const float* __restrict__ Wor,
     const float* __restrict__ x,
     const int* __restrict__ eptr, const int* __restrict__ ecnt,
-    const int* __restrict__ eperm, float* __restrict__ tN, int Nn)
+    const int* __restrict__ eperm, float* __restrict__ tN)
 {
     const int lane = threadIdx.x & 63;
-    int wid = (blockIdx.x * blockDim.x + threadIdx.x) >> 6;
-    const int nw = (gridDim.x * blockDim.x) >> 6;
+    int wid = bx * 4 + (threadIdx.x >> 6);
+    const int nw = nblk * 4;
     float wr0[NRAD], wr1[NRAD];
     #pragma unroll
     for (int k = 0; k < NRAD; ++k) {
         wr0[k] = Wor[k * H_DIM + lane];
         wr1[k] = Wor[k * H_DIM + lane + 64];
     }
-    for (int n = wid; n < Nn; n += nw) {
+    for (int n = wid; n < N_NODES; n += nw) {
         int start = eptr[n];
         int end   = start + ecnt[n];
         float a0 = 0.f, a1 = 0.f;
@@ -860,6 +767,122 @@
         }
         tN[(size_t)n * H_DIM + lane] = a0;
         tN[(size_t)n * H_DIM + lane + 64] = a1;
+    }
+}
+
+__global__ __launch_bounds__(256) void gather_fused(
+    int GT,
+    const u16* __restrict__ ps8b, const float* __restrict__ Wsb2,
+    const float* __restrict__ xkj, const int* __restrict__ pkj,
+    const int* __restrict__ tptr, const int* __restrict__ tcnt,
+    float* __restrict__ agg,
+    const float* __restrict__ rbf, const float* __restrict__ Wor,
+    const float* __restrict__ x,
+    const int* __restrict__ eptr, const int* __restrict__ ecnt,
+    const int* __restrict__ eperm, float* __restrict__ tN)
+{
+    int bx = blockIdx.x;
+    if (bx < GT)
+        triplet_body(bx, GT, ps8b, Wsb2, xkj, pkj, tptr, tcnt, agg);
+    else
+        out_gather_body(bx - GT, gridDim.x - GT, rbf, Wor, x, eptr, ecnt, eperm, tN);
+}
+
+__global__ __launch_bounds__(256) void csr_count(
+    const int* __restrict__ idx, int* __restrict__ cnt, int n)
+{
+    int i = blockIdx.x * 256 + threadIdx.x;
+    if (i < n) atomicAdd(&cnt[idx[i]], 1);
+}
+
+__global__ __launch_bounds__(256) void scan_block(
+    const int* __restrict__ cnt, int* __restrict__ ptr, int* __restrict__ bsum, int n)
+{
+    __shared__ int s[256];
+    int i = blockIdx.x * 256 + threadIdx.x;
+    int v = (i < n) ? cnt[i] : 0;
+    s[threadIdx.x] = v;
+    __syncthreads();
+    #pragma unroll
+    for (int off = 1; off < 256; off <<= 1) {
+        int t = (threadIdx.x >= off) ? s[threadIdx.x - off] : 0;
+        __syncthreads();
+        s[threadIdx.x] += t;
+        __syncthreads();
+    }
+    if (i < n) ptr[i] = s[threadIdx.x] - v;
+    if (threadIdx.x == 255) bsum[blockIdx.x] = s[255];
+}
+
+__global__ __launch_bounds__(1024) void scan_aux(int* __restrict__ bsum, int nb)
+{
+    __shared__ int s[1024];
+    int v = (threadIdx.x < nb) ? bsum[threadIdx.x] : 0;
+    s[threadIdx.x] = v;
+    __syncthreads();
+    #pragma unroll
+    for (int off = 1; off < 1024; off <<= 1) {
+        int t = (threadIdx.x >= off) ? s[threadIdx.x - off] : 0;
+        __syncthreads();
+        s[threadIdx.x] += t;
+        __syncthreads();
+    }
+    if (threadIdx.x < nb) bsum[threadIdx.x] = s[threadIdx.x] - v;
+}
+
+__global__ __launch_bounds__(256) void scan_add(
+    int* __restrict__ ptr, const int* __restrict__ bsum, int n)
+{
+    int i = blockIdx.x * 256 + threadIdx.x;
+    if (i < n) ptr[i] += bsum[blockIdx.x];
+}
+
+__global__ __launch_bounds__(256) void csr_fill(
+    const int* __restrict__ idx, int* __restrict__ cursor,
+    int* __restrict__ perm, int n)
+{
+    int i = blockIdx.x * 256 + threadIdx.x;
+    if (i >= n) return;
+    int pos = atomicAdd(&cursor[idx[i]], 1);
+    perm[pos] = i;
+}
+
+__global__ __launch_bounds__(256) void permute_s8(
+    const float* __restrict__ sbf, const float* __restrict__ W1all,
+    const int* __restrict__ idx_kj, const int* __restrict__ tperm,
+    u16* __restrict__ ps8, int* __restrict__ pkj, int Tcount)
+{
+    __shared__ float Ws[NB * SBF_D * BAS];
+    for (int i = threadIdx.x; i < NB * SBF_D * BAS; i += 256) Ws[i] = W1all[i];
+    __syncthreads();
+    int i = blockIdx.x * 256 + threadIdx.x;
+    if (i >= Tcount) return;
+    int t = tperm[i];
+    pkj[i] = idx_kj[t];
+    float s[SBF_D];
+    {
+        const float2* p2 = reinterpret_cast<const float2*>(&sbf[(size_t)t * SBF_D]);
+        #pragma unroll
+        for (int k = 0; k < SBF_D / 2; ++k) {
+            float2 v = p2[k];
+            s[2 * k] = v.x; s[2 * k + 1] = v.y;
+        }
+    }
+    #pragma unroll
+    for (int b = 0; b < NB; ++b) {
+        const float* Wb_ = &Ws[b * SBF_D * BAS];
+        float acc[BAS] = {};
+        for (int k = 0; k < SBF_D; ++k) {
+            float sv = s[k];
+            #pragma unroll
+            for (int j = 0; j < BAS; ++j)
+                acc[j] = fmaf(sv, Wb_[k * BAS + j], acc[j]);
+        }
+        ushort4 o0 = make_ushort4(f2bf(acc[0]), f2bf(acc[1]), f2bf(acc[2]), f2bf(acc[3]));
+        ushort4 o1 = make_ushort4(f2bf(acc[4]), f2bf(acc[5]), f2bf(acc[6]), f2bf(acc[7]));
+        u16* op = &ps8[((size_t)b * Tcount + i) * BAS];
+        *reinterpret_cast<ushort4*>(op) = o0;
+        *reinterpret_cast<ushort4*>(op + 4) = o1;
     }
 }
 
@@ -908,7 +931,6 @@
     float* E1 = (float*)alloc((size_t)E_EDGES * H_DIM * 4);
     float* C1 = (float*)alloc((size_t)E_EDGES * INT_DIM * 4);
     float* C2 = (float*)alloc((size_t)E_EDGES * INT_DIM * 4);
-    float* R8 = (float*)alloc((size_t)E_EDGES * BAS * 4);
     float* TN = (float*)alloc((size_t)N_NODES * H_DIM * 4);
     u16* HKJ = (u16*)alloc(4  * 16384 * 2); u16* LKJ = (u16*)alloc(4  * 16384 * 2);
     u16* HJI = (u16*)alloc(4  * 16384 * 2); u16* LJI = (u16*)alloc(4  * 16384 * 2);
@@ -977,41 +999,40 @@
     float* P = (float*)d_out;
     hipMemsetAsync(P, 0, (size_t)N_NODES * sizeof(float), stream);
 
-    auto out_block = [&](int ob, const float* xcur) {
-        hipLaunchKernelGGL(out_gather, dim3(2048), dim3(256), 0, stream,
-                           rbf, Wo_rbf + (size_t)ob * NRAD * H_DIM, xcur,
-                           eptr, ecnt, eperm, TN, N_NODES);
-        hipLaunchKernelGGL(out_chain, dim3(N_NODES / 32), dim3(256), 0, stream,
-                           TN,
-                           HOU + (size_t)ob * 32768, LOU + (size_t)ob * 32768,
-                           bo_up + (size_t)ob * OUT_EMB,
-                           HOL + (size_t)(ob * 3 + 0) * 65536, LOL + (size_t)(ob * 3 + 0) * 65536,
-                           bo_lins + (size_t)(ob * 3 + 0) * OUT_EMB,
-                           HOL + (size_t)(ob * 3 + 1) * 65536, LOL + (size_t)(ob * 3 + 1) * 65536,
-                           bo_lins + (size_t)(ob * 3 + 1) * OUT_EMB,
-                           HOL + (size_t)(ob * 3 + 2) * 65536, LOL + (size_t)(ob * 3 + 2) * 65536,
-                           bo_lins + (size_t)(ob * 3 + 2) * OUT_EMB,
-                           Wo_out + (size_t)ob * OUT_EMB, P);
+    auto make_outp = [&](int ob) {
+        OutP o;
+        o.TN = TN;
+        o.Uh = HOU + (size_t)ob * 32768; o.Ul = LOU + (size_t)ob * 32768;
+        o.bu = bo_up + (size_t)ob * OUT_EMB;
+        o.L0h = HOL + (size_t)(ob * 3 + 0) * 65536; o.L0l = LOL + (size_t)(ob * 3 + 0) * 65536;
+        o.b0 = bo_lins + (size_t)(ob * 3 + 0) * OUT_EMB;
+        o.L1h = HOL + (size_t)(ob * 3 + 1) * 65536; o.L1l = LOL + (size_t)(ob * 3 + 1) * 65536;
+        o.b1 = bo_lins + (size_t)(ob * 3 + 1) * OUT_EMB;
+        o.L2h = HOL + (size_t)(ob * 3 + 2) * 65536; o.L2l = LOL + (size_t)(ob * 3 + 2) * 65536;
+        o.b2 = bo_lins + (size_t)(ob * 3 + 2) * OUT_EMB;
+        o.Wo = Wo_out + (size_t)ob * OUT_EMB;
+        o.P = P;
+        return o;
     };
-
-    out_block(0, x_in);
 
     const float* xcur = x_in;
     const int EB = E_EDGES / 64;
+    const int GT = 2048;
     for (int b = 0; b < NB; ++b) {
         float* xnext = (b % 2 == 0) ? XB : XA;
-        hipLaunchKernelGGL(rbf8_kernel, dim3((E_EDGES + 255) / 256), dim3(256), 0, stream,
-                           rbf, W_rbf1 + (size_t)b * NRAD * BAS, R8, E_EDGES);
         hipLaunchKernelGGL(pre_fuse, dim3(EB), dim3(256), 0, stream,
-                           xcur, R8,
+                           xcur, rbf, W_rbf1 + (size_t)b * NRAD * BAS,
                            HJI + (size_t)b * 16384, LJI + (size_t)b * 16384, b_ji + (size_t)b * H_DIM,
                            HKJ + (size_t)b * 16384, LKJ + (size_t)b * 16384, b_kj + (size_t)b * H_DIM,
                            W_rbf2 + (size_t)b * BAS * H_DIM,
                            HDN + (size_t)b * 8192, LDN + (size_t)b * 8192,
                            E1, C1);
-        hipLaunchKernelGGL(triplet_gather2, dim3(2048), dim3(256), 0, stream,
+        hipLaunchKernelGGL(gather_fused, dim3(GT + 2048), dim3(256), 0, stream,
+                           GT,
                            PS8 + (size_t)b * T_TRIP * BAS, W_sbf2 + (size_t)b * BAS * INT_DIM,
-                           C1, PKJ, tptr, tcnt, C2, E_EDGES);
+                           C1, PKJ, tptr, tcnt, C2,
+                           rbf, Wo_rbf + (size_t)b * NRAD * H_DIM, xcur,
+                           eptr, ecnt, eperm, TN);
         ChainP cp;
         cp.uph = HUP + (size_t)b * 8192;  cp.upl = LUP + (size_t)b * 8192;
         cp.b0h = HWB + (size_t)(b * 2 + 0) * 16384; cp.b0l = LWB + (size_t)(b * 2 + 0) * 16384;
@@ -1028,9 +1049,20 @@
         cp.ba1 = ba + (size_t)(b * 4 + 1) * H_DIM;
         cp.ba2 = ba + (size_t)(b * 4 + 2) * H_DIM;
         cp.ba3 = ba + (size_t)(b * 4 + 3) * H_DIM;
-        hipLaunchKernelGGL(post_chain, dim3(EB), dim3(256), 0, stream,
-                           C2, E1, xcur, cp, xnext);
+        OutP op = make_outp(b);
+        hipLaunchKernelGGL(post_fused, dim3(EB + N_NODES / 32), dim3(256), 0, stream,
+                           EB, C2, E1, xcur, cp, xnext, op);
         xcur = xnext;
-        out_block(b + 1, xcur);
-    }
-}
+    }
+    {
+        OutP op = make_outp(NB);
+        ChainP cp = {};
+        hipLaunchKernelGGL(gather_fused, dim3(2048), dim3(256), 0, stream,
+                           0,
+                           PS8, W_sbf2, C1, PKJ, tptr, tcnt, C2,
+                           rbf, Wo_rbf + (size_t)NB * NRAD * H_DIM, xcur,
+                           eptr, ecnt, eperm, TN);
+        hipLaunchKernelGGL(post_fused, dim3(N_NODES / 32), dim3(256), 0, stream,
+                           0, C2, E1, xcur, cp, (float*)XA, op);
+    }
+}
```

Result: faster. 4.168 ms (-4.7%).
